# Optimization experiments

Measured on AMD Instinct MI355X. Metric: run time of the kernel, lower is better.

## Reference

```python
import jax, jax.numpy as jnp
import numpy as np

# Structural metadata (constants): 3 node types, 4 edge types, 2 HGT layers.
T, R, L = 3, 4, 2
H_HID, HEADS, OUT = 256, 8, 128
D = H_HID // HEADS  # per-head dim = 32
SRC_T = (0, 1, 1, 1)  # (author->paper, paper->author, paper->paper, paper->venue)
DST_T = (1, 0, 1, 2)
LN_EPS = 1e-5


def _segment_softmax(logits, seg, n):
    # logits: [E, heads]; softmax over edges sharing the same destination node
    m = jax.ops.segment_max(logits, seg, num_segments=n)
    e = jnp.exp(logits - m[seg])
    s = jax.ops.segment_sum(e, seg, num_segments=n)
    return e / s[seg]


def setup_inputs() -> dict:
    key = jax.random.key(0)
    ks = iter(jax.random.split(key, 64))
    N, E, FIN = 20000, 60000, 128

    def nrm(shape, scale):
        return jax.random.normal(next(ks), shape, jnp.float32) * scale

    return dict(
        x=jax.random.normal(next(ks), (T, N, FIN), jnp.float32),
        edge_index=jax.random.randint(next(ks), (R, 2, E), 0, N),
        Win=nrm((T, FIN, H_HID), 0.05),
        b_in=jnp.zeros((T, H_HID), jnp.float32),
        Wk=nrm((L, T, H_HID, H_HID), 0.05), bk=jnp.zeros((L, T, H_HID), jnp.float32),
        Wq=nrm((L, T, H_HID, H_HID), 0.05), bq=jnp.zeros((L, T, H_HID), jnp.float32),
        Wv=nrm((L, T, H_HID, H_HID), 0.05), bv=jnp.zeros((L, T, H_HID), jnp.float32),
        Wa=nrm((L, T, H_HID, H_HID), 0.05), ba=jnp.zeros((L, T, H_HID), jnp.float32),
        skip=jnp.ones((L, T), jnp.float32),
        a_rel=nrm((L, R, HEADS, D, D), 0.1),
        m_rel=nrm((L, R, HEADS, D, D), 0.1),
        p_rel=jnp.ones((L, R, HEADS), jnp.float32),
        ln_g=jnp.ones((L, T, H_HID), jnp.float32),
        ln_b=jnp.zeros((L, T, H_HID), jnp.float32),
        Wout=nrm((H_HID, OUT), 0.05),
        bout=jnp.zeros((OUT,), jnp.float32),
    )


def reference(x, edge_index, Win, b_in, Wk, bk, Wq, bq, Wv, bv, Wa, ba,
              skip, a_rel, m_rel, p_rel, ln_g, ln_b, Wout, bout):
    N = x.shape[1]
    inv_sqrt_d = jnp.float32(1.0 / np.sqrt(D))
    # Input projection + ReLU (dropout = identity in eval mode)
    h = jax.nn.relu(jnp.einsum('tnf,tfh->tnh', x, Win) + b_in[:, None, :])

    for l in range(L):
        res = h
        # Per-node-type k/q/v projections, reshaped to heads
        k = (jnp.einsum('tnh,tho->tno', h, Wk[l]) + bk[l][:, None]).reshape(T, N, HEADS, D)
        q = (jnp.einsum('tnh,tho->tno', h, Wq[l]) + bq[l][:, None]).reshape(T, N, HEADS, D)
        v = (jnp.einsum('tnh,tho->tno', h, Wv[l]) + bv[l][:, None]).reshape(T, N, HEADS, D)

        agg = jnp.zeros((T, N, HEADS, D), h.dtype)
        for r in range(R):
            st, dt = SRC_T[r], DST_T[r]
            src, dst = edge_index[r, 0], edge_index[r, 1]
            # Per-edge-type relation transforms on source k/v
            k_r = jnp.einsum('nhd,hde->nhe', k[st], a_rel[l, r])
            v_r = jnp.einsum('nhd,hde->nhe', v[st], m_rel[l, r])
            kj = k_r[src]          # [E, heads, d]
            vj = v_r[src]
            qi = q[dt][dst]
            logits = (qi * kj).sum(-1) * p_rel[l, r] * inv_sqrt_d  # [E, heads]
            alpha = _segment_softmax(logits, dst, N)
            msg = vj * alpha[..., None]
            agg = agg.at[dt].add(jax.ops.segment_sum(msg, dst, num_segments=N))

        # Type-specific output linear after exact GELU, gated skip (in==out dims)
        o = jax.nn.gelu(agg.reshape(T, N, H_HID), approximate=False)
        o = jnp.einsum('tnh,tho->tno', o, Wa[l]) + ba[l][:, None]
        beta = jax.nn.sigmoid(skip[l])[:, None, None]
        h = beta * o + (1.0 - beta) * h

        # Model-level residual + LayerNorm + ReLU (dropout = identity)
        h = h + res
        mu = h.mean(-1, keepdims=True)
        var = ((h - mu) ** 2).mean(-1, keepdims=True)
        h = (h - mu) * jax.lax.rsqrt(var + LN_EPS) * ln_g[l][:, None] + ln_b[l][:, None]
        h = jax.nn.relu(h)

    # Shared output projection; outputs stacked over node types: [T, N, OUT]
    return jnp.einsum('tnh,ho->tno', h, Wout) + bout
```

## Files before the change

kernel.cpp:

```cpp
#include <hip/hip_runtime.h>
#include <math.h>

#define T_ 3
#define R_ 4
#define L_ 2
#define H_ 256
#define HEADS_ 8
#define D_ 32
#define FIN_ 128
#define OUT_ 128

typedef unsigned short bf16_t;
typedef __attribute__((ext_vector_type(8))) short bf16x8;
typedef __attribute__((ext_vector_type(4))) float f32x4;

__device__ __forceinline__ float bf2f(bf16_t h) {
    return __uint_as_float(((unsigned)h) << 16);
}
__device__ __forceinline__ bf16_t f2bf(float f) {
    unsigned u = __float_as_uint(f);
    u += 0x7FFFu + ((u >> 16) & 1u);
    return (bf16_t)(u >> 16);
}
__device__ __forceinline__ float gelu_exact(float x) {
    return 0.5f * x * (1.0f + erff(x * 0.70710678118654752440f));
}

__global__ void zero_kernel(unsigned* __restrict__ p, long n) {
    long i = (long)blockIdx.x * blockDim.x + threadIdx.x;
    long stride = (long)gridDim.x * blockDim.x;
    for (; i < n; i += stride) p[i] = 0u;
}

__global__ __launch_bounds__(256) void transconv2_kernel(
    const float* __restrict__ in0, bf16_t* __restrict__ out0,
    const float* __restrict__ in1, bf16_t* __restrict__ out1,
    int cnt0, int Rr, int Cc)
{
    __shared__ float Ls[64][65];
    const int tid = threadIdx.x;
    int z = blockIdx.z;
    const float* in;
    bf16_t* out;
    if (z < cnt0) { in = in0; out = out0; }
    else          { in = in1; out = out1; z -= cnt0; }
    const long base = (long)z * Rr * Cc;
    const int r0 = blockIdx.y * 64, c0 = blockIdx.x * 64;
    #pragma unroll
    for (int i = 0; i < 16; ++i) {
        int e = tid + i * 256; int row = e >> 6, col = e & 63;
        Ls[row][col] = in[base + (long)(r0 + row) * Cc + c0 + col];
    }
    __syncthreads();
    #pragma unroll
    for (int i = 0; i < 16; ++i) {
        int e = tid + i * 256; int row = e >> 6, col = e & 63;
        out[base + (long)(c0 + row) * Rr + r0 + col] = f2bf(Ls[col][row]);
    }
}

__global__ __launch_bounds__(256) void transconv_kernel(
    const float* __restrict__ in, bf16_t* __restrict__ out, int Rr, int Cc)
{
    __shared__ float Ls[64][65];
    const int tid = threadIdx.x;
    const long base = (long)blockIdx.z * Rr * Cc;
    const int r0 = blockIdx.y * 64, c0 = blockIdx.x * 64;
    #pragma unroll
    for (int i = 0; i < 16; ++i) {
        int e = tid + i * 256; int row = e >> 6, col = e & 63;
        Ls[row][col] = in[base + (long)(r0 + row) * Cc + c0 + col];
    }
    __syncthreads();
    #pragma unroll
    for (int i = 0; i < 16; ++i) {
        int e = tid + i * 256; int row = e >> 6, col = e & 63;
        out[base + (long)(c0 + row) * Rr + r0 + col] = f2bf(Ls[col][row]);
    }
}

__global__ __launch_bounds__(256) void fuse_wT_kernel(
    const float* __restrict__ Wk, const float* __restrict__ Wv,
    const float* __restrict__ bk, const float* __restrict__ bv,
    const float* __restrict__ a_rel, const float* __restrict__ m_rel,
    bf16_t* __restrict__ WkvT, float* __restrict__ bkv)
{
    const int s = blockIdx.z;
    const int kv = s & 1, r = (s >> 1) & 3, l = s >> 3;
    const int SRCT[4] = {0, 1, 1, 1};
    const int st = SRCT[r];
    const float* W = (kv ? Wv : Wk) + ((long)l * T_ + st) * H_ * H_;
    const float* A = (kv ? m_rel : a_rel) + ((long)l * R_ + r) * HEADS_ * D_ * D_;
    const int hh = blockIdx.y, kt = blockIdx.x;
    __shared__ float As[32][33];
    __shared__ float Ws[64][33];
    const int tid = threadIdx.x;
    {
        int d = tid >> 3, e4 = (tid & 7) * 4;
        float4 v = *(const float4*)(A + (hh * D_ + d) * D_ + e4);
        As[d][e4] = v.x; As[d][e4 + 1] = v.y; As[d][e4 + 2] = v.z; As[d][e4 + 3] = v.w;
    }
    #pragma unroll
    for (int p = 0; p < 2; ++p) {
        int idx = p * 256 + tid;
        int row = idx >> 3, c4 = (idx & 7) * 4;
        float4 v = *(const float4*)(W + (long)(kt * 64 + row) * H_ + hh * 32 + c4);
        Ws[row][c4] = v.x; Ws[row][c4 + 1] = v.y; Ws[row][c4 + 2] = v.z; Ws[row][c4 + 3] = v.w;
    }
    __syncthreads();
    const int kl = tid & 63, eb = tid >> 6;
    #pragma unroll
    for (int ii = 0; ii < 8; ++ii) {
        int e = eb * 8 + ii;
        float acc = 0.f;
        #pragma unroll
        for (int d = 0; d < 32; ++d)
            acc += As[d][e] * Ws[kl][d];
        long rowIdx = (long)(s >> 1) * 512 + (kv * 256) + hh * 32 + e;
        WkvT[rowIdx * H_ + kt * 64 + kl] = f2bf(acc);
    }
    if (blockIdx.x == 0 && blockIdx.y == 0) {
        const float* b = (kv ? bv : bk) + ((long)l * T_ + st) * H_;
        const int bh = tid >> 5, be = tid & 31;
        float acc = 0.f;
        #pragma unroll
        for (int d = 0; d < D_; ++d)
            acc += b[bh * D_ + d] * A[(bh * D_ + d) * D_ + be];
        bkv[(long)(s >> 1) * 512 + kv * 256 + tid] = acc;
    }
}

__global__ void hist_kernel(const int* __restrict__ ei, int* __restrict__ indeg,
                            int Nn, int E)
{
    int idx = blockIdx.x * 256 + threadIdx.x;
    if (idx >= R_ * E) return;
    int r = idx / E, e = idx - r * E;
    int d = ei[(size_t)r * 2 * E + E + e];
    atomicAdd(indeg + (size_t)r * Nn + d, 1);
}

__global__ __launch_bounds__(256) void csr_part_kernel(
    const int* __restrict__ indeg, int* __restrict__ partials, int Nn, int nch)
{
    const int r = blockIdx.y, c = blockIdx.x, tid = threadIdx.x;
    const int lane = tid & 63, wave = tid >> 6;
    int idx = c * 256 + tid;
    int v = (idx < Nn) ? indeg[(size_t)r * Nn + idx] : 0;
    #pragma unroll
    for (int off = 1; off < 64; off <<= 1) v += __shfl_xor(v, off);
    __shared__ int wsum[4];
    if (lane == 0) wsum[wave] = v;
    __syncthreads();
    if (tid == 0) partials[r * nch + c] = wsum[0] + wsum[1] + wsum[2] + wsum[3];
}

__global__ __launch_bounds__(256) void csr_scanpart_kernel(
    int* __restrict__ partials, int nch)
{
    const int r = blockIdx.x, tid = threadIdx.x;
    __shared__ int sh[256];
    int v = (tid < nch) ? partials[r * nch + tid] : 0;
    sh[tid] = v;
    __syncthreads();
    for (int off = 1; off < 256; off <<= 1) {
        int u = (tid >= off) ? sh[tid - off] : 0;
        __syncthreads();
        sh[tid] += u;
        __syncthreads();
    }
    if (tid < nch) partials[r * nch + tid] = sh[tid] - v;
}

__global__ __launch_bounds__(256) void csr_write_kernel(
    const int* __restrict__ indeg, const int* __restrict__ partials,
    int* __restrict__ offs, int* __restrict__ cursor, int Nn, int nch)
{
    const int r = blockIdx.y, c = blockIdx.x, tid = threadIdx.x;
    int idx = c * 256 + tid;
    int v = (idx < Nn) ? indeg[(size_t)r * Nn + idx] : 0;
    __shared__ int sh[256];
    sh[tid] = v;
    __syncthreads();
    for (int off = 1; off < 256; off <<= 1) {
        int u = (tid >= off) ? sh[tid - off] : 0;
        __syncthreads();
        sh[tid] += u;
        __syncthreads();
    }
    int incl = sh[tid];
    int base = partials[r * nch + c];
    if (idx < Nn) {
        int excl = base + incl - v;
        offs[(size_t)r * (Nn + 1) + idx] = excl;
        cursor[(size_t)r * Nn + idx] = excl;
        if (idx == Nn - 1) offs[(size_t)r * (Nn + 1) + Nn] = base + incl;
    }
}

__global__ void scatter_kernel(const int* __restrict__ ei, int* __restrict__ cursor,
                               int* __restrict__ esrc, int Nn, int E)
{
    int idx = blockIdx.x * 256 + threadIdx.x;
    if (idx >= R_ * E) return;
    int r = idx / E, e = idx - r * E;
    int s = ei[(size_t)r * 2 * E + e];
    int d = ei[(size_t)r * 2 * E + E + e];
    int pos = atomicAdd(cursor + (size_t)r * Nn + d, 1);
    esrc[(size_t)r * E + pos] = s;
}

__global__ __launch_bounds__(256) void agg_all_kernel(
    const int* __restrict__ offs, const int* __restrict__ esrc,
    bf16_t* __restrict__ qbuf, const bf16_t* __restrict__ KV,
    const float* __restrict__ p_l, float scale, int Nn, int E)
{
    static const int NRELg[3] = {2, 1, 1};
    static const int R0g[3]  = {0, 1, 3};
    static const int R1g[3]  = {2, 0, 0};
    static const int DTg[3]  = {1, 0, 2};
    const int grp = blockIdx.y;
    const int wave = threadIdx.x >> 6, lane = threadIdx.x & 63;
    const int d = blockIdx.x * 4 + wave;
    if (d >= Nn) return;
    const int head = lane >> 3;
    const int dt = DTg[grp];

    bf16_t* qrow = qbuf + (size_t)dt * Nn * H_ + (size_t)d * H_;
    ushort4 qu = ((const ushort4*)qrow)[lane];
    float q0 = bf2f(qu.x), q1 = bf2f(qu.y), q2 = bf2f(qu.z), q3 = bf2f(qu.w);

    const int rA = R0g[grp];
    const int* esA = esrc + (size_t)rA * E;
    const bf16_t* kvA = KV + (size_t)rA * Nn * 512;
    float prA = p_l[rA * HEADS_ + head] * scale;
    int curA = offs[(size_t)rA * (Nn + 1) + d];
    int endA = offs[(size_t)rA * (Nn + 1) + d + 1];

    const int* esB; const bf16_t* kvB; float prB;
    int curB, endB;
    const bool separate = (NRELg[grp] == 2);
    if (separate) {
        const int rB = R1g[grp];
        esB = esrc + (size_t)rB * E;
        kvB = KV + (size_t)rB * Nn * 512;
        prB = p_l[rB * HEADS_ + head] * scale;
        curB = offs[(size_t)rB * (Nn + 1) + d];
        endB = offs[(size_t)rB * (Nn + 1) + d + 1];
    } else {
        int mid = curA + ((endA - curA + 1) >> 1);
        esB = esA; kvB = kvA; prB = prA;
        curB = mid; endB = endA;
        endA = mid;
    }

    float mA = -INFINITY, sA = 0.f, aA0 = 0.f, aA1 = 0.f, aA2 = 0.f, aA3 = 0.f;
    float mB = -INFINITY, sB = 0.f, aB0 = 0.f, aB1 = 0.f, aB2 = 0.f, aB3 = 0.f;

    while (curA < endA || curB < endB) {
        const bool hA = curA < endA, hB = curB < endB;
        ushort4 kuA, vuA, kuB, vuB;
        if (hA) {
            const bf16_t* row = kvA + (size_t)esA[curA] * 512;
            kuA = ((const ushort4*)row)[lane];
            vuA = ((const ushort4*)(row + 256))[lane];
        }
        if (hB) {
            const bf16_t* row = kvB + (size_t)esB[curB] * 512;
            kuB = ((const ushort4*)row)[lane];
            vuB = ((const ushort4*)(row + 256))[lane];
        }
        if (hA) {
            float dt_ = q0 * bf2f(kuA.x) + q1 * bf2f(kuA.y) + q2 * bf2f(kuA.z) + q3 * bf2f(kuA.w);
            dt_ += __shfl_xor(dt_, 1);
            dt_ += __shfl_xor(dt_, 2);
            dt_ += __shfl_xor(dt_, 4);
            float lg = dt_ * prA;
            float mnew = fmaxf(mA, lg);
            float fac = __expf(mA - mnew);
            float p = __expf(lg - mnew);
            sA = sA * fac + p;
            aA0 = aA0 * fac + p * bf2f(vuA.x);
            aA1 = aA1 * fac + p * bf2f(vuA.y);
            aA2 = aA2 * fac + p * bf2f(vuA.z);
            aA3 = aA3 * fac + p * bf2f(vuA.w);
            mA = mnew;
            ++curA;
        }
        if (hB) {
            float dt_ = q0 * bf2f(kuB.x) + q1 * bf2f(kuB.y) + q2 * bf2f(kuB.z) + q3 * bf2f(kuB.w);
            dt_ += __shfl_xor(dt_, 1);
            dt_ += __shfl_xor(dt_, 2);
            dt_ += __shfl_xor(dt_, 4);
            float lg = dt_ * prB;
            float mnew = fmaxf(mB, lg);
            float fac = __expf(mB - mnew);
            float p = __expf(lg - mnew);
            sB = sB * fac + p;
            aB0 = aB0 * fac + p * bf2f(vuB.x);
            aB1 = aB1 * fac + p * bf2f(vuB.y);
            aB2 = aB2 * fac + p * bf2f(vuB.z);
            aB3 = aB3 * fac + p * bf2f(vuB.w);
            mB = mnew;
            ++curB;
        }
    }

    float t0, t1, t2, t3;
    if (separate) {
        float iA = (sA > 0.f) ? 1.f / sA : 0.f;
        float iB = (sB > 0.f) ? 1.f / sB : 0.f;
        t0 = aA0 * iA + aB0 * iB;
        t1 = aA1 * iA + aB1 * iB;
        t2 = aA2 * iA + aB2 * iB;
        t3 = aA3 * iA + aB3 * iB;
    } else {
        if (sB > 0.f) {
            float m = fmaxf(mA, mB);
            float fA = (sA > 0.f) ? __expf(mA - m) : 0.f;
            float fB = __expf(mB - m);
            sA = sA * fA + sB * fB;
            aA0 = aA0 * fA + aB0 * fB;
            aA1 = aA1 * fA + aB1 * fB;
            aA2 = aA2 * fA + aB2 * fB;
            aA3 = aA3 * fA + aB3 * fB;
        }
        float iA = (sA > 0.f) ? 1.f / sA : 0.f;
        t0 = aA0 * iA; t1 = aA1 * iA; t2 = aA2 * iA; t3 = aA3 * iA;
    }
    ushort4 ou;
    ou.x = f2bf(gelu_exact(t0));
    ou.y = f2bf(gelu_exact(t1));
    ou.z = f2bf(gelu_exact(t2));
    ou.w = f2bf(gelu_exact(t3));
    ((ushort4*)qrow)[lane] = ou;
}

#define ASTR 40
#define ESTR 72

template<typename TA, typename TC, int ACT_C>
__global__ __launch_bounds__(256) void mfma_gemm(
    const TA* __restrict__ A, const TA* __restrict__ A2, int zsplit,
    const bf16_t* __restrict__ BT,
    const float* __restrict__ bias, TC* __restrict__ C,
    int M, int K, int Nc,
    long strideA, long strideB, long strideBias, long strideC)
{
    const int gX = gridDim.x, gY = gridDim.y, gZ = gridDim.z;
    const int nwg = gX * gY * gZ;
    int flat = blockIdx.x + gX * (blockIdx.y + gY * blockIdx.z);
    const int qch = nwg >> 3, rch = nwg & 7;
    int xcd = flat & 7, cidx = flat >> 3;
    int swz = (xcd < rch ? xcd * (qch + 1) : rch * (qch + 1) + (xcd - rch) * qch) + cidx;
    const int by = swz / (gX * gZ);
    int rem = swz - by * (gX * gZ);
    const int bz = rem / gX;
    const int bx = rem - bz * gX;

    const TA* Ab = (bz < zsplit) ? (A + (long)bz * strideA) : A2;
    const bf16_t* Bb = BT + (long)bz * strideB;
    const float* biasb = bias + (long)bz * strideBias;
    TC* Cb = C + (long)bz * strideC;

    __shared__ bf16_t As[128 * ASTR];
    __shared__ bf16_t Bs[128 * ASTR];
    __shared__ bf16_t Es[4 * 16 * ESTR];
    const int tid = threadIdx.x;
    const int lane = tid & 63, wave = tid >> 6;
    const int wr = wave >> 1, wc = wave & 1;
    const int bm = by * 128, bn = bx * 128;
    const int r16 = lane & 15, g = lane >> 4;
    f32x4 acc[4][4] = {};

    for (int k0 = 0; k0 < K; k0 += 32) {
        #pragma unroll
        for (int p = 0; p < 2; ++p) {
            int idx = p * 256 + tid;
            int row = idx >> 2, seg = idx & 3;
            int grow = bm + row;
            bf16x8 av = {};
            if (grow < M) {
                if constexpr (sizeof(TA) == 2) {
                    av = *(const bf16x8*)(Ab + (long)grow * K + k0 + seg * 8);
                } else {
                    const float* sp = (const float*)Ab + (long)grow * K + k0 + seg * 8;
                    float4 f0 = *(const float4*)sp, f1 = *(const float4*)(sp + 4);
                    av[0] = (short)f2bf(f0.x); av[1] = (short)f2bf(f0.y);
                    av[2] = (short)f2bf(f0.z); av[3] = (short)f2bf(f0.w);
                    av[4] = (short)f2bf(f1.x); av[5] = (short)f2bf(f1.y);
                    av[6] = (short)f2bf(f1.z); av[7] = (short)f2bf(f1.w);
                }
            }
            *(bf16x8*)(As + row * ASTR + seg * 8) = av;
            bf16x8 bv = *(const bf16x8*)(Bb + (long)(bn + row) * K + k0 + seg * 8);
            *(bf16x8*)(Bs + row * ASTR + seg * 8) = bv;
        }
        __syncthreads();
        bf16x8 af[4], bfr[4];
        #pragma unroll
        for (int m = 0; m < 4; ++m)
            af[m] = *(const bf16x8*)(As + (wr * 64 + m * 16 + r16) * ASTR + g * 8);
        #pragma unroll
        for (int n = 0; n < 4; ++n)
            bfr[n] = *(const bf16x8*)(Bs + (wc * 64 + n * 16 + r16) * ASTR + g * 8);
        #pragma unroll
        for (int m = 0; m < 4; ++m)
            #pragma unroll
            for (int n = 0; n < 4; ++n)
                acc[m][n] = __builtin_amdgcn_mfma_f32_16x16x32_bf16(af[m], bfr[n], acc[m][n], 0, 0, 0);
        __syncthreads();
    }

    float bb[4];
    #pragma unroll
    for (int n = 0; n < 4; ++n)
        bb[n] = biasb[bn + wc * 64 + n * 16 + r16];

    if constexpr (sizeof(TC) == 2) {
        bf16_t* st = Es + wave * (16 * ESTR);
        #pragma unroll
        for (int m = 0; m < 4; ++m) {
            int rowbase = bm + wr * 64 + m * 16;
            #pragma unroll
            for (int n = 0; n < 4; ++n) {
                #pragma unroll
                for (int j = 0; j < 4; ++j) {
                    float vv = acc[m][n][j] + bb[n];
                    if (ACT_C) vv = fmaxf(vv, 0.f);
                    st[(g * 4 + j) * ESTR + n * 16 + r16] = f2bf(vv);
                }
            }
            #pragma unroll
            for (int p = 0; p < 2; ++p) {
                int row = p * 8 + (lane >> 3);
                int col0 = (lane & 7) * 8;
                int grow = rowbase + row;
                bf16x8 val = *(const bf16x8*)(st + row * ESTR + col0);
                if (grow < M)
                    *(bf16x8*)(Cb + (long)grow * Nc + bn + wc * 64 + col0) = val;
            }
        }
    } else {
        #pragma unroll
        for (int n = 0; n < 4; ++n) {
            int col = bn + wc * 64 + n * 16 + r16;
            #pragma unroll
            for (int m = 0; m < 4; ++m) {
                int rowbase = bm + wr * 64 + m * 16 + g * 4;
                #pragma unroll
                for (int j = 0; j < 4; ++j) {
                    int row = rowbase + j;
                    if (row < M) {
                        float vv = acc[m][n][j] + bb[n];
                        if (ACT_C) vv = fmaxf(vv, 0.f);
                        Cb[(long)row * Nc + col] = vv;
                    }
                }
            }
        }
    }
}

__global__ __launch_bounds__(256) void skip_ln_kernel(
    bf16_t* __restrict__ h, const bf16_t* __restrict__ o,
    const float* __restrict__ skip, const float* __restrict__ ln_g,
    const float* __restrict__ ln_b, int Nn)
{
    const int wave = threadIdx.x >> 6;
    const int lane = threadIdx.x & 63;
    long row = (long)blockIdx.x * 4 + wave;
    long total = (long)T_ * Nn;
    if (row >= total) return;
    int t = (int)(row / Nn);
    float beta = 1.f / (1.f + expf(-skip[t]));
    float cb = 2.f - beta;
    ushort4 hv = reinterpret_cast<const ushort4*>(h + row * H_)[lane];
    ushort4 ov = reinterpret_cast<const ushort4*>(o + row * H_)[lane];
    float u0 = beta * bf2f(ov.x) + cb * bf2f(hv.x);
    float u1 = beta * bf2f(ov.y) + cb * bf2f(hv.y);
    float u2 = beta * bf2f(ov.z) + cb * bf2f(hv.z);
    float u3 = beta * bf2f(ov.w) + cb * bf2f(hv.w);
    float s1 = u0 + u1 + u2 + u3;
    float s2 = u0 * u0 + u1 * u1 + u2 * u2 + u3 * u3;
    #pragma unroll
    for (int off = 1; off < 64; off <<= 1) {
        s1 += __shfl_xor(s1, off);
        s2 += __shfl_xor(s2, off);
    }
    float mu = s1 * (1.f / H_);
    float var = s2 * (1.f / H_) - mu * mu;
    float inv = rsqrtf(var + 1e-5f);
    const float4 g = reinterpret_cast<const float4*>(ln_g + (size_t)t * H_)[lane];
    const float4 b = reinterpret_cast<const float4*>(ln_b + (size_t)t * H_)[lane];
    ushort4 r;
    r.x = f2bf(fmaxf((u0 - mu) * inv * g.x + b.x, 0.f));
    r.y = f2bf(fmaxf((u1 - mu) * inv * g.y + b.y, 0.f));
    r.z = f2bf(fmaxf((u2 - mu) * inv * g.z + b.z, 0.f));
    r.w = f2bf(fmaxf((u3 - mu) * inv * g.w + b.w, 0.f));
    reinterpret_cast<ushort4*>(h + row * H_)[lane] = r;
}

extern "C" void kernel_launch(void* const* d_in, const int* in_sizes, int n_in,
                              void* d_out, int out_size, void* d_ws, size_t ws_size,
                              hipStream_t stream)
{
    const float* x     = (const float*)d_in[0];
    const int*   ei    = (const int*)  d_in[1];
    const float* Win   = (const float*)d_in[2];
    const float* b_in  = (const float*)d_in[3];
    const float* Wk    = (const float*)d_in[4];
    const float* bk    = (const float*)d_in[5];
    const float* Wq    = (const float*)d_in[6];
    const float* bq    = (const float*)d_in[7];
    const float* Wv    = (const float*)d_in[8];
    const float* bv    = (const float*)d_in[9];
    const float* Wa    = (const float*)d_in[10];
    const float* ba    = (const float*)d_in[11];
    const float* skip  = (const float*)d_in[12];
    const float* a_rel = (const float*)d_in[13];
    const float* m_rel = (const float*)d_in[14];
    const float* p_rel = (const float*)d_in[15];
    const float* ln_g  = (const float*)d_in[16];
    const float* ln_b  = (const float*)d_in[17];
    const float* Wout  = (const float*)d_in[18];
    const float* bout  = (const float*)d_in[19];
    float* out = (float*)d_out;

    const int N = in_sizes[0] / (T_ * FIN_);
    const int E = in_sizes[1] / (R_ * 2);
    const size_t NH = (size_t)N * H_;
    const int nch = (N + 255) / 256;
    const int ZBIG = 1 << 20;

    char* wp = (char*)d_ws;
    auto alloc = [&](size_t bytes) {
        void* r = wp;
        wp += (bytes + 255) & ~(size_t)255;
        return r;
    };
    bf16_t* h     = (bf16_t*)alloc(T_ * NH * 2);
    bf16_t* qbuf  = (bf16_t*)alloc(T_ * NH * 2);
    bf16_t* KV    = (bf16_t*)alloc((size_t)R_ * N * 512 * 2);
    int*    indeg = (int*)   alloc((size_t)R_ * N * 4);
    int*    offs  = (int*)   alloc((size_t)R_ * (N + 1) * 4);
    int*    cursor= (int*)   alloc((size_t)R_ * N * 4);
    int*    esrc  = (int*)   alloc((size_t)R_ * E * 4);
    int*    parts = (int*)   alloc((size_t)R_ * 256 * 4);
    bf16_t* WqT   = (bf16_t*)alloc((size_t)L_ * T_ * H_ * H_ * 2);
    bf16_t* WaT   = (bf16_t*)alloc((size_t)L_ * T_ * H_ * H_ * 2);
    bf16_t* WinT  = (bf16_t*)alloc((size_t)T_ * FIN_ * H_ * 2);
    bf16_t* WoutT = (bf16_t*)alloc((size_t)H_ * OUT_ * 2);
    bf16_t* WkvT  = (bf16_t*)alloc((size_t)L_ * R_ * 512 * H_ * 2);
    float*  bkv   = (float*) alloc((size_t)L_ * R_ * 512 * 4);

    bf16_t* obuf = KV;

    if ((size_t)(wp - (char*)d_ws) > ws_size) return;

    const float scale = 0.17677669529663688f;
    dim3 blk(256);
    auto gM = [](long M) { return (int)((M + 127) / 128); };

    transconv2_kernel<<<dim3(4, 4, 2 * L_ * T_), blk, 0, stream>>>(
        Wq, WqT, Wa, WaT, L_ * T_, H_, H_);
    transconv_kernel<<<dim3(4, 2, T_), blk, 0, stream>>>(Win, WinT, FIN_, H_);
    transconv_kernel<<<dim3(2, 4, 1),  blk, 0, stream>>>(Wout, WoutT, H_, OUT_);
    fuse_wT_kernel<<<dim3(4, 8, 16), blk, 0, stream>>>(
        Wk, Wv, bk, bv, a_rel, m_rel, WkvT, bkv);

    zero_kernel<<<256, blk, 0, stream>>>((unsigned*)indeg, (long)R_ * N);
    hist_kernel<<<(R_ * E + 255) / 256, blk, 0, stream>>>(ei, indeg, N, E);
    csr_part_kernel<<<dim3(nch, R_), blk, 0, stream>>>(indeg, parts, N, nch);
    csr_scanpart_kernel<<<R_, blk, 0, stream>>>(parts, nch);
    csr_write_kernel<<<dim3(nch, R_), blk, 0, stream>>>(indeg, parts, offs, cursor, N, nch);
    scatter_kernel<<<(R_ * E + 255) / 256, blk, 0, stream>>>(ei, cursor, esrc, N, E);

    mfma_gemm<float, bf16_t, 1><<<dim3(H_ / 128, gM(N), T_), blk, 0, stream>>>(
        x, x, ZBIG, WinT, b_in, h, N, FIN_, H_,
        (long)N * FIN_, (long)FIN_ * H_, H_, (long)NH);

    for (int l = 0; l < L_; ++l) {
        const long lw = (long)l * R_;
        mfma_gemm<bf16_t, bf16_t, 0><<<dim3(512 / 128, gM(N), 4), blk, 0, stream>>>(
            h, h + NH, 1, WkvT + lw * 512 * H_, bkv + lw * 512, KV,
            N, H_, 512, 0L, 512L * H_, 512L, (long)N * 512);
        mfma_gemm<bf16_t, bf16_t, 0><<<dim3(H_ / 128, gM(N), 3), blk, 0, stream>>>(
            h, h, ZBIG, WqT + (size_t)l * T_ * H_ * H_, bq + (size_t)l * T_ * H_, qbuf,
            N, H_, H_, (long)NH, (long)H_ * H_, (long)H_, (long)NH);
        agg_all_kernel<<<dim3((N + 3) / 4, 3), blk, 0, stream>>>(
            offs, esrc, qbuf, KV, p_rel + (size_t)l * R_ * HEADS_, scale, N, E);
        mfma_gemm<bf16_t, bf16_t, 0><<<dim3(H_ / 128, gM(N), 3), blk, 0, stream>>>(
            qbuf, qbuf, ZBIG, WaT + (size_t)l * T_ * H_ * H_, ba + (size_t)l * T_ * H_, obuf,
            N, H_, H_, (long)NH, (long)H_ * H_, (long)H_, (long)NH);
        skip_ln_kernel<<<((size_t)T_ * N + 3) / 4, blk, 0, stream>>>(
            h, obuf, skip + l * T_, ln_g + (size_t)l * T_ * H_, ln_b + (size_t)l * T_ * H_, N);
    }

    mfma_gemm<bf16_t, float, 0><<<dim3(OUT_ / 128, gM((long)T_ * N), 1), blk, 0, stream>>>(
        h, h, ZBIG, WoutT, bout, out, T_ * N, H_, OUT_, 0L, 0L, 0L, 0L);
}
```

Measured before the change: 410.7 us.

## Split edge aggregation into four concurrent online-softmax chains with lazy rescaling

Result: slower. 482.1 us (+17.4%).

```diff
diff --git a/kernel.cpp b/kernel.cpp
--- a/kernel.cpp
+++ b/kernel.cpp
@@ -16,6 +16,12 @@
 
 __device__ __forceinline__ float bf2f(bf16_t h) {
     return __uint_as_float(((unsigned)h) << 16);
+}
+__device__ __forceinline__ float bflo(unsigned u) {
+    return __uint_as_float(u << 16);
+}
+__device__ __forceinline__ float bfhi(unsigned u) {
+    return __uint_as_float(u & 0xffff0000u);
 }
 __device__ __forceinline__ bf16_t f2bf(float f) {
     unsigned u = __float_as_uint(f);
@@ -207,8 +213,21 @@
     int s = ei[(size_t)r * 2 * E + e];
     int d = ei[(size_t)r * 2 * E + E + e];
     int pos = atomicAdd(cursor + (size_t)r * Nn + d, 1);
-    esrc[(size_t)r * E + pos] = s;
-}
+    esrc[(size_t)r * E + pos] = s * 512;
+}
+
+#define MERGE(X, Y)                                                     \
+    {                                                                   \
+        float mm = fmaxf(m[X], m[Y]);                                   \
+        float fx = (s[X] > 0.f) ? __expf(m[X] - mm) : 0.f;              \
+        float fy = (s[Y] > 0.f) ? __expf(m[Y] - mm) : 0.f;              \
+        s[X] = s[X] * fx + s[Y] * fy;                                   \
+        a0[X] = a0[X] * fx + a0[Y] * fy;                                \
+        a1[X] = a1[X] * fx + a1[Y] * fy;                                \
+        a2[X] = a2[X] * fx + a2[Y] * fy;                                \
+        a3[X] = a3[X] * fx + a3[Y] * fy;                                \
+        m[X] = mm;                                                      \
+    }
 
 __global__ __launch_bounds__(256) void agg_all_kernel(
     const int* __restrict__ offs, const int* __restrict__ esrc,
@@ -225,108 +244,111 @@
     if (d >= Nn) return;
     const int head = lane >> 3;
     const int dt = DTg[grp];
-
-    bf16_t* qrow = qbuf + (size_t)dt * Nn * H_ + (size_t)d * H_;
-    ushort4 qu = ((const ushort4*)qrow)[lane];
-    float q0 = bf2f(qu.x), q1 = bf2f(qu.y), q2 = bf2f(qu.z), q3 = bf2f(qu.w);
-
-    const int rA = R0g[grp];
-    const int* esA = esrc + (size_t)rA * E;
-    const bf16_t* kvA = KV + (size_t)rA * Nn * 512;
-    float prA = p_l[rA * HEADS_ + head] * scale;
-    int curA = offs[(size_t)rA * (Nn + 1) + d];
-    int endA = offs[(size_t)rA * (Nn + 1) + d + 1];
-
-    const int* esB; const bf16_t* kvB; float prB;
-    int curB, endB;
     const bool separate = (NRELg[grp] == 2);
-    if (separate) {
-        const int rB = R1g[grp];
-        esB = esrc + (size_t)rB * E;
-        kvB = KV + (size_t)rB * Nn * 512;
-        prB = p_l[rB * HEADS_ + head] * scale;
-        curB = offs[(size_t)rB * (Nn + 1) + d];
-        endB = offs[(size_t)rB * (Nn + 1) + d + 1];
-    } else {
-        int mid = curA + ((endA - curA + 1) >> 1);
-        esB = esA; kvB = kvA; prB = prA;
-        curB = mid; endB = endA;
-        endA = mid;
-    }
-
-    float mA = -INFINITY, sA = 0.f, aA0 = 0.f, aA1 = 0.f, aA2 = 0.f, aA3 = 0.f;
-    float mB = -INFINITY, sB = 0.f, aB0 = 0.f, aB1 = 0.f, aB2 = 0.f, aB3 = 0.f;
-
-    while (curA < endA || curB < endB) {
-        const bool hA = curA < endA, hB = curB < endB;
-        ushort4 kuA, vuA, kuB, vuB;
-        if (hA) {
-            const bf16_t* row = kvA + (size_t)esA[curA] * 512;
-            kuA = ((const ushort4*)row)[lane];
-            vuA = ((const ushort4*)(row + 256))[lane];
+
+    bf16_t* qrow = qbuf + ((size_t)dt * Nn + d) * H_;
+    uint2 qu = ((const uint2*)qrow)[lane];
+    float q0 = bflo(qu.x), q1 = bfhi(qu.x), q2 = bflo(qu.y), q3 = bfhi(qu.y);
+
+    const int* es[4];
+    const bf16_t* kv[4];
+    float pr[4];
+    int cur[4], end[4];
+
+    {
+        const int rA = R0g[grp];
+        const int* esA = esrc + (size_t)rA * E;
+        const bf16_t* kvA = KV + (size_t)rA * Nn * 512;
+        float prA = p_l[rA * HEADS_ + head] * scale;
+        int bA = offs[(size_t)rA * (Nn + 1) + d];
+        int eA = offs[(size_t)rA * (Nn + 1) + d + 1];
+        if (separate) {
+            const int rB = R1g[grp];
+            const int* esB = esrc + (size_t)rB * E;
+            const bf16_t* kvB = KV + (size_t)rB * Nn * 512;
+            float prB = p_l[rB * HEADS_ + head] * scale;
+            int bB = offs[(size_t)rB * (Nn + 1) + d];
+            int eB = offs[(size_t)rB * (Nn + 1) + d + 1];
+            int mA = bA + ((eA - bA + 1) >> 1);
+            int mB = bB + ((eB - bB + 1) >> 1);
+            es[0] = esA; kv[0] = kvA; pr[0] = prA; cur[0] = bA; end[0] = mA;
+            es[1] = esA; kv[1] = kvA; pr[1] = prA; cur[1] = mA; end[1] = eA;
+            es[2] = esB; kv[2] = kvB; pr[2] = prB; cur[2] = bB; end[2] = mB;
+            es[3] = esB; kv[3] = kvB; pr[3] = prB; cur[3] = mB; end[3] = eB;
+        } else {
+            int n = eA - bA;
+            int c1 = bA + (n * 1) / 4, c2 = bA + (n * 2) / 4, c3 = bA + (n * 3) / 4;
+            es[0] = esA; kv[0] = kvA; pr[0] = prA; cur[0] = bA; end[0] = c1;
+            es[1] = esA; kv[1] = kvA; pr[1] = prA; cur[1] = c1; end[1] = c2;
+            es[2] = esA; kv[2] = kvA; pr[2] = prA; cur[2] = c2; end[2] = c3;
+            es[3] = esA; kv[3] = kvA; pr[3] = prA; cur[3] = c3; end[3] = eA;
         }
-        if (hB) {
-            const bf16_t* row = kvB + (size_t)esB[curB] * 512;
-            kuB = ((const ushort4*)row)[lane];
-            vuB = ((const ushort4*)(row + 256))[lane];
+    }
+
+    float m[4], s[4], a0[4], a1[4], a2[4], a3[4];
+    #pragma unroll
+    for (int c = 0; c < 4; ++c) {
+        m[c] = -INFINITY; s[c] = 0.f;
+        a0[c] = 0.f; a1[c] = 0.f; a2[c] = 0.f; a3[c] = 0.f;
+    }
+
+    for (;;) {
+        bool h[4];
+        bool anyh = false;
+        #pragma unroll
+        for (int c = 0; c < 4; ++c) { h[c] = cur[c] < end[c]; anyh |= h[c]; }
+        if (!anyh) break;
+        uint2 ku[4], vu[4];
+        #pragma unroll
+        for (int c = 0; c < 4; ++c) if (h[c]) {
+            const bf16_t* row = kv[c] + es[c][cur[c]];
+            ku[c] = ((const uint2*)row)[lane];
+            vu[c] = ((const uint2*)(row + 256))[lane];
         }
-        if (hA) {
-            float dt_ = q0 * bf2f(kuA.x) + q1 * bf2f(kuA.y) + q2 * bf2f(kuA.z) + q3 * bf2f(kuA.w);
+        #pragma unroll
+        for (int c = 0; c < 4; ++c) if (h[c]) {
+            float dt_ = q0 * bflo(ku[c].x) + q1 * bfhi(ku[c].x)
+                      + q2 * bflo(ku[c].y) + q3 * bfhi(ku[c].y);
             dt_ += __shfl_xor(dt_, 1);
             dt_ += __shfl_xor(dt_, 2);
             dt_ += __shfl_xor(dt_, 4);
-            float lg = dt_ * prA;
-            float mnew = fmaxf(mA, lg);
-            float fac = __expf(mA - mnew);
-            float p = __expf(lg - mnew);
-            sA = sA * fac + p;
-            aA0 = aA0 * fac + p * bf2f(vuA.x);
-            aA1 = aA1 * fac + p * bf2f(vuA.y);
-            aA2 = aA2 * fac + p * bf2f(vuA.z);
-            aA3 = aA3 * fac + p * bf2f(vuA.w);
-            mA = mnew;
-            ++curA;
+            float lg = dt_ * pr[c];
+            if (__any(lg - m[c] > 8.f)) {
+                float mn = fmaxf(m[c], lg);
+                float fac = __expf(m[c] - mn);
+                float p = __expf(lg - mn);
+                s[c] = s[c] * fac + p;
+                a0[c] = a0[c] * fac + p * bflo(vu[c].x);
+                a1[c] = a1[c] * fac + p * bfhi(vu[c].x);
+                a2[c] = a2[c] * fac + p * bflo(vu[c].y);
+                a3[c] = a3[c] * fac + p * bfhi(vu[c].y);
+                m[c] = mn;
+            } else {
+                float p = __expf(lg - m[c]);
+                s[c] += p;
+                a0[c] += p * bflo(vu[c].x);
+                a1[c] += p * bfhi(vu[c].x);
+                a2[c] += p * bflo(vu[c].y);
+                a3[c] += p * bfhi(vu[c].y);
+            }
+            ++cur[c];
         }
-        if (hB) {
-            float dt_ = q0 * bf2f(kuB.x) + q1 * bf2f(kuB.y) + q2 * bf2f(kuB.z) + q3 * bf2f(kuB.w);
-            dt_ += __shfl_xor(dt_, 1);
-            dt_ += __shfl_xor(dt_, 2);
-            dt_ += __shfl_xor(dt_, 4);
-            float lg = dt_ * prB;
-            float mnew = fmaxf(mB, lg);
-            float fac = __expf(mB - mnew);
-            float p = __expf(lg - mnew);
-            sB = sB * fac + p;
-            aB0 = aB0 * fac + p * bf2f(vuB.x);
-            aB1 = aB1 * fac + p * bf2f(vuB.y);
-            aB2 = aB2 * fac + p * bf2f(vuB.z);
-            aB3 = aB3 * fac + p * bf2f(vuB.w);
-            mB = mnew;
-            ++curB;
-        }
-    }
-
+    }
+
+    MERGE(0, 1)
+    MERGE(2, 3)
     float t0, t1, t2, t3;
     if (separate) {
-        float iA = (sA > 0.f) ? 1.f / sA : 0.f;
-        float iB = (sB > 0.f) ? 1.f / sB : 0.f;
-        t0 = aA0 * iA + aB0 * iB;
-        t1 = aA1 * iA + aB1 * iB;
-        t2 = aA2 * iA + aB2 * iB;
-        t3 = aA3 * iA + aB3 * iB;
+        float iA = (s[0] > 0.f) ? 1.f / s[0] : 0.f;
+        float iB = (s[2] > 0.f) ? 1.f / s[2] : 0.f;
+        t0 = a0[0] * iA + a0[2] * iB;
+        t1 = a1[0] * iA + a1[2] * iB;
+        t2 = a2[0] * iA + a2[2] * iB;
+        t3 = a3[0] * iA + a3[2] * iB;
     } else {
-        if (sB > 0.f) {
-            float m = fmaxf(mA, mB);
-            float fA = (sA > 0.f) ? __expf(mA - m) : 0.f;
-            float fB = __expf(mB - m);
-            sA = sA * fA + sB * fB;
-            aA0 = aA0 * fA + aB0 * fB;
-            aA1 = aA1 * fA + aB1 * fB;
-            aA2 = aA2 * fA + aB2 * fB;
-            aA3 = aA3 * fA + aB3 * fB;
-        }
-        float iA = (sA > 0.f) ? 1.f / sA : 0.f;
-        t0 = aA0 * iA; t1 = aA1 * iA; t2 = aA2 * iA; t3 = aA3 * iA;
+        MERGE(0, 2)
+        float iA = (s[0] > 0.f) ? 1.f / s[0] : 0.f;
+        t0 = a0[0] * iA; t1 = a1[0] * iA; t2 = a2[0] * iA; t3 = a3[0] * iA;
     }
     ushort4 ou;
     ou.x = f2bf(gelu_exact(t0));
```

## Prefetch next edge KV rows and use lazy max rescaling in aggregation

Applied to the files above, without the earlier changes.

Measured after the change: 412.8 us. About the same (+0.5%).

```diff
diff --git a/kernel.cpp b/kernel.cpp
--- a/kernel.cpp
+++ b/kernel.cpp
@@ -16,6 +16,12 @@
 
 __device__ __forceinline__ float bf2f(bf16_t h) {
     return __uint_as_float(((unsigned)h) << 16);
+}
+__device__ __forceinline__ float bflo(unsigned u) {
+    return __uint_as_float(u << 16);
+}
+__device__ __forceinline__ float bfhi(unsigned u) {
+    return __uint_as_float(u & 0xffff0000u);
 }
 __device__ __forceinline__ bf16_t f2bf(float f) {
     unsigned u = __float_as_uint(f);
@@ -207,10 +213,38 @@
     int s = ei[(size_t)r * 2 * E + e];
     int d = ei[(size_t)r * 2 * E + E + e];
     int pos = atomicAdd(cursor + (size_t)r * Nn + d, 1);
-    esrc[(size_t)r * E + pos] = s;
-}
-
-__global__ __launch_bounds__(256) void agg_all_kernel(
+    esrc[(size_t)r * E + pos] = s * 512;
+}
+
+#define CHAIN_STEP(ku, vu, prX, mX, sX, x0, x1, x2, x3)                     \
+    {                                                                        \
+        float dt_ = q0 * bflo(ku.x) + q1 * bfhi(ku.x)                        \
+                  + q2 * bflo(ku.y) + q3 * bfhi(ku.y);                       \
+        dt_ += __shfl_xor(dt_, 1);                                           \
+        dt_ += __shfl_xor(dt_, 2);                                           \
+        dt_ += __shfl_xor(dt_, 4);                                           \
+        float lg = dt_ * prX;                                                \
+        if (__any(lg - mX > 8.f)) {                                          \
+            float mn = fmaxf(mX, lg);                                        \
+            float fac = __expf(mX - mn);                                     \
+            float p = __expf(lg - mn);                                       \
+            sX = sX * fac + p;                                               \
+            x0 = x0 * fac + p * bflo(vu.x);                                  \
+            x1 = x1 * fac + p * bfhi(vu.x);                                  \
+            x2 = x2 * fac + p * bflo(vu.y);                                  \
+            x3 = x3 * fac + p * bfhi(vu.y);                                  \
+            mX = mn;                                                         \
+        } else {                                                             \
+            float p = __expf(lg - mX);                                       \
+            sX += p;                                                         \
+            x0 += p * bflo(vu.x);                                            \
+            x1 += p * bfhi(vu.x);                                            \
+            x2 += p * bflo(vu.y);                                            \
+            x3 += p * bfhi(vu.y);                                            \
+        }                                                                    \
+    }
+
+__global__ __launch_bounds__(512) void agg_all_kernel(
     const int* __restrict__ offs, const int* __restrict__ esrc,
     bf16_t* __restrict__ qbuf, const bf16_t* __restrict__ KV,
     const float* __restrict__ p_l, float scale, int Nn, int E)
@@ -221,14 +255,15 @@
     static const int DTg[3]  = {1, 0, 2};
     const int grp = blockIdx.y;
     const int wave = threadIdx.x >> 6, lane = threadIdx.x & 63;
-    const int d = blockIdx.x * 4 + wave;
+    const int d = blockIdx.x * 8 + wave;
     if (d >= Nn) return;
     const int head = lane >> 3;
     const int dt = DTg[grp];
-
-    bf16_t* qrow = qbuf + (size_t)dt * Nn * H_ + (size_t)d * H_;
-    ushort4 qu = ((const ushort4*)qrow)[lane];
-    float q0 = bf2f(qu.x), q1 = bf2f(qu.y), q2 = bf2f(qu.z), q3 = bf2f(qu.w);
+    const bool separate = (NRELg[grp] == 2);
+
+    bf16_t* qrow = qbuf + ((size_t)dt * Nn + d) * H_;
+    uint2 qu = ((const uint2*)qrow)[lane];
+    float q0 = bflo(qu.x), q1 = bfhi(qu.x), q2 = bflo(qu.y), q3 = bfhi(qu.y);
 
     const int rA = R0g[grp];
     const int* esA = esrc + (size_t)rA * E;
@@ -239,7 +274,6 @@
 
     const int* esB; const bf16_t* kvB; float prB;
     int curB, endB;
-    const bool separate = (NRELg[grp] == 2);
     if (separate) {
         const int rB = R1g[grp];
         esB = esrc + (size_t)rB * E;
@@ -257,53 +291,33 @@
     float mA = -INFINITY, sA = 0.f, aA0 = 0.f, aA1 = 0.f, aA2 = 0.f, aA3 = 0.f;
     float mB = -INFINITY, sB = 0.f, aB0 = 0.f, aB1 = 0.f, aB2 = 0.f, aB3 = 0.f;
 
-    while (curA < endA || curB < endB) {
-        const bool hA = curA < endA, hB = curB < endB;
-        ushort4 kuA, vuA, kuB, vuB;
-        if (hA) {
-            const bf16_t* row = kvA + (size_t)esA[curA] * 512;
-            kuA = ((const ushort4*)row)[lane];
-            vuA = ((const ushort4*)(row + 256))[lane];
+    bool hA = curA < endA, hB = curB < endB;
+    uint2 kA, vA, kB, vB;
+    if (hA) {
+        const bf16_t* r = kvA + esA[curA];
+        kA = ((const uint2*)r)[lane]; vA = ((const uint2*)(r + 256))[lane];
+    }
+    if (hB) {
+        const bf16_t* r = kvB + esB[curB];
+        kB = ((const uint2*)r)[lane]; vB = ((const uint2*)(r + 256))[lane];
+    }
+
+    while (hA || hB) {
+        bool nA = hA && (curA + 1 < endA);
+        bool nB = hB && (curB + 1 < endB);
+        uint2 kA2, vA2, kB2, vB2;
+        if (nA) {
+            const bf16_t* r = kvA + esA[curA + 1];
+            kA2 = ((const uint2*)r)[lane]; vA2 = ((const uint2*)(r + 256))[lane];
         }
-        if (hB) {
-            const bf16_t* row = kvB + (size_t)esB[curB] * 512;
-            kuB = ((const ushort4*)row)[lane];
-            vuB = ((const ushort4*)(row + 256))[lane];
+        if (nB) {
+            const bf16_t* r = kvB + esB[curB + 1];
+            kB2 = ((const uint2*)r)[lane]; vB2 = ((const uint2*)(r + 256))[lane];
         }
-        if (hA) {
-            float dt_ = q0 * bf2f(kuA.x) + q1 * bf2f(kuA.y) + q2 * bf2f(kuA.z) + q3 * bf2f(kuA.w);
-            dt_ += __shfl_xor(dt_, 1);
-            dt_ += __shfl_xor(dt_, 2);
-            dt_ += __shfl_xor(dt_, 4);
-            float lg = dt_ * prA;
-            float mnew = fmaxf(mA, lg);
-            float fac = __expf(mA - mnew);
-            float p = __expf(lg - mnew);
-            sA = sA * fac + p;
-            aA0 = aA0 * fac + p * bf2f(vuA.x);
-            aA1 = aA1 * fac + p * bf2f(vuA.y);
-            aA2 = aA2 * fac + p * bf2f(vuA.z);
-            aA3 = aA3 * fac + p * bf2f(vuA.w);
-            mA = mnew;
-            ++curA;
-        }
-        if (hB) {
-            float dt_ = q0 * bf2f(kuB.x) + q1 * bf2f(kuB.y) + q2 * bf2f(kuB.z) + q3 * bf2f(kuB.w);
-            dt_ += __shfl_xor(dt_, 1);
-            dt_ += __shfl_xor(dt_, 2);
-            dt_ += __shfl_xor(dt_, 4);
-            float lg = dt_ * prB;
-            float mnew = fmaxf(mB, lg);
-            float fac = __expf(mB - mnew);
-            float p = __expf(lg - mnew);
-            sB = sB * fac + p;
-            aB0 = aB0 * fac + p * bf2f(vuB.x);
-            aB1 = aB1 * fac + p * bf2f(vuB.y);
-            aB2 = aB2 * fac + p * bf2f(vuB.z);
-            aB3 = aB3 * fac + p * bf2f(vuB.w);
-            mB = mnew;
-            ++curB;
-        }
+        if (hA) { CHAIN_STEP(kA, vA, prA, mA, sA, aA0, aA1, aA2, aA3) ++curA; }
+        if (hB) { CHAIN_STEP(kB, vB, prB, mB, sB, aB0, aB1, aB2, aB3) ++curB; }
+        kA = kA2; vA = vA2; kB = kB2; vB = vB2;
+        hA = nA; hB = nB;
     }
 
     float t0, t1, t2, t3;
@@ -316,14 +330,14 @@
         t3 = aA3 * iA + aB3 * iB;
     } else {
         if (sB > 0.f) {
-            float m = fmaxf(mA, mB);
-            float fA = (sA > 0.f) ? __expf(mA - m) : 0.f;
-            float fB = __expf(mB - m);
-            sA = sA * fA + sB * fB;
-            aA0 = aA0 * fA + aB0 * fB;
-            aA1 = aA1 * fA + aB1 * fB;
-            aA2 = aA2 * fA + aB2 * fB;
-            aA3 = aA3 * fA + aB3 * fB;
+            float mm = fmaxf(mA, mB);
+            float fx = (sA > 0.f) ? __expf(mA - mm) : 0.f;
+            float fy = __expf(mB - mm);
+            sA = sA * fx + sB * fy;
+            aA0 = aA0 * fx + aB0 * fy;
+            aA1 = aA1 * fx + aB1 * fy;
+            aA2 = aA2 * fx + aB2 * fy;
+            aA3 = aA3 * fx + aB3 * fy;
         }
         float iA = (sA > 0.f) ? 1.f / sA : 0.f;
         t0 = aA0 * iA; t1 = aA1 * iA; t2 = aA2 * iA; t3 = aA3 * iA;
@@ -588,7 +602,7 @@
         mfma_gemm<bf16_t, bf16_t, 0><<<dim3(H_ / 128, gM(N), 3), blk, 0, stream>>>(
             h, h, ZBIG, WqT + (size_t)l * T_ * H_ * H_, bq + (size_t)l * T_ * H_, qbuf,
             N, H_, H_, (long)NH, (long)H_ * H_, (long)H_, (long)NH);
-        agg_all_kernel<<<dim3((N + 3) / 4, 3), blk, 0, stream>>>(
+        agg_all_kernel<<<dim3((N + 7) / 8, 3), dim3(512), 0, stream>>>(
             offs, esrc, qbuf, KV, p_rel + (size_t)l * R_ * HEADS_, scale, N, E);
         mfma_gemm<bf16_t, bf16_t, 0><<<dim3(H_ / 128, gM(N), 3), blk, 0, stream>>>(
             qbuf, qbuf, ZBIG, WaT + (size_t)l * T_ * H_ * H_, ba + (size_t)l * T_ * H_, obuf,
```
